# Optimization experiments

Measured on AMD Instinct MI355X. Metric: run time of the kernel, lower is better.

## Reference

```python
import jax, jax.numpy as jnp
import numpy as np

EPS = 1e-5

def conv1x1(x, w, b):
    # x: [B,C,H,W], w: [O,C], b: [O]
    return jnp.einsum('bchw,oc->bohw', x, w) + b[None, :, None, None]

def bn(x, gamma, beta, mean, var):
    scale = gamma / jnp.sqrt(var + EPS)
    return x * scale[None, :, None, None] + (beta - mean * scale)[None, :, None, None]

def setup_inputs() -> dict:
    B, C, H, W = 8, 256, 64, 64
    F0, F1 = 128, 128
    key = jax.random.key(0)
    ks = jax.random.split(key, 16)
    d = {}
    d['inputs'] = jax.random.normal(ks[0], (B, C, H, W), dtype=jnp.float32)
    def make_cna(i, fout, fin):
        w = jax.random.normal(ks[i], (fout, fin), dtype=jnp.float32) / np.sqrt(fin)
        b = jnp.zeros((fout,), dtype=jnp.float32)
        g = jnp.ones((fout,), dtype=jnp.float32)
        be = jnp.zeros((fout,), dtype=jnp.float32)
        m = 0.1 * jax.random.normal(ks[i + 1], (fout,), dtype=jnp.float32)
        v = jax.random.uniform(ks[i + 2], (fout,), dtype=jnp.float32, minval=0.5, maxval=1.5)
        return w, b, g, be, m, v
    (d['theta_w'], d['theta_b'], d['theta_g'], d['theta_beta'], d['theta_m'], d['theta_v']) = make_cna(1, F0, C)
    (d['phi_w'], d['phi_b'], d['phi_g'], d['phi_beta'], d['phi_m'], d['phi_v']) = make_cna(4, F0, C)
    (d['mu_w'], d['mu_b'], d['mu_g'], d['mu_beta'], d['mu_m'], d['mu_v']) = make_cna(7, F1, C)
    d['pre_w'] = jax.random.normal(ks[10], (C, F1), dtype=jnp.float32) / np.sqrt(F1)
    d['pre_b'] = jnp.zeros((C,), dtype=jnp.float32)
    d['post_g'] = jnp.ones((C,), dtype=jnp.float32)
    d['post_beta'] = jnp.zeros((C,), dtype=jnp.float32)
    d['post_m'] = 0.1 * jax.random.normal(ks[11], (C,), dtype=jnp.float32)
    d['post_v'] = jax.random.uniform(ks[12], (C,), dtype=jnp.float32, minval=0.5, maxval=1.5)
    return d

def reference(inputs, theta_w, theta_b, theta_g, theta_beta, theta_m, theta_v,
              phi_w, phi_b, phi_g, phi_beta, phi_m, phi_v,
              mu_w, mu_b, mu_g, mu_beta, mu_m, mu_v,
              pre_w, pre_b, post_g, post_beta, post_m, post_v):
    B, C, H, W = inputs.shape
    N = H * W
    # theta/phi/mu: 1x1 conv + batchnorm (eval) + relu
    t = jax.nn.relu(bn(conv1x1(inputs, theta_w, theta_b), theta_g, theta_beta, theta_m, theta_v))
    p = jax.nn.relu(bn(conv1x1(inputs, phi_w, phi_b), phi_g, phi_beta, phi_m, phi_v))
    z = jax.nn.relu(bn(conv1x1(inputs, mu_w, mu_b), mu_g, mu_beta, mu_m, mu_v))
    tf = t.reshape(B, -1, N)   # [B,F0,N]
    pf = p.reshape(B, -1, N)   # [B,F0,N]
    zf = z.reshape(B, -1, N)   # [B,F1,N]
    # unscaled softmax(theta^T phi) mu^T, batched (original loops over B)
    attn = jax.nn.softmax(jnp.einsum('bfn,bfm->bnm', tf, pf), axis=-1)  # [B,N,N]
    u = jnp.einsum('bnm,bfm->bfn', attn, zf).reshape(B, -1, H, W)       # [B,F1,H,W]
    pre = conv1x1(u, pre_w, pre_b)                                       # [B,C,H,W]
    return jax.nn.relu(bn(pre + inputs, post_g, post_beta, post_m, post_v))
```

## Files before the change

kernel.cpp:

```cpp
#include <hip/hip_runtime.h>

typedef __attribute__((ext_vector_type(8))) _Float16 f16x8;
typedef __attribute__((ext_vector_type(4))) float f32x4;

#define EPSV 1e-5f
#define BB 8
#define CC 256
#define NP 4096
#define FF 128
#define SPLIT 4
#define CHUNK 1024

static __device__ __forceinline__ unsigned short f2h(float f) {
    union { _Float16 h; unsigned short u; } v;
    v.h = (_Float16)f;
    return v.u;
}
static __device__ __forceinline__ float h2f(unsigned short u) {
    union { unsigned short u; _Float16 h; } v;
    v.u = u;
    return (float)v.h;
}

struct PrepArgs {
    const float* w[3]; const float* bias[3]; const float* g[3]; const float* be[3];
    const float* m[3]; const float* v[3];
    const float* pre_w; const float* pre_b;
    const float* post_g; const float* post_be; const float* post_m; const float* post_v;
    unsigned short* W_all; float* b_all; unsigned short* W2; float* b2; float* sres;
};

__global__ __launch_bounds__(256) void prep_kernel(PrepArgs a) {
    int idx = blockIdx.x * 256 + threadIdx.x;
    if (idx < 3 * 128 * 256) {
        int row = idx >> 8, c = idx & 255;
        int which = row >> 7, f = row & 127;
        float s = a.g[which][f] * rsqrtf(a.v[which][f] + EPSV);
        a.W_all[idx] = f2h(a.w[which][f * 256 + c] * s);
        if (c == 0)
            a.b_all[row] = s * a.bias[which][f] + a.be[which][f] - a.m[which][f] * s;
    } else {
        int i = idx - 3 * 128 * 256;
        if (i < 256 * 128) {
            int c = i >> 7, f = i & 127;
            float s = a.post_g[c] * rsqrtf(a.post_v[c] + EPSV);
            a.W2[i] = f2h(a.pre_w[i] * s);
            if (f == 0) {
                a.b2[c] = s * a.pre_b[c] + a.post_be[c] - a.post_m[c] * s;
                a.sres[c] = s;
            }
        }
    }
}

__global__ __launch_bounds__(256) void transpose_x_kernel(const float* __restrict__ x,
                                                          unsigned short* __restrict__ xT) {
    __shared__ float tile[64][65];
    int blk = blockIdx.x;
    int b  = blk >> 8;
    int c0 = ((blk >> 6) & 3) << 6;
    int n0 = (blk & 63) << 6;
    int t = threadIdx.x;
    const float* src = x + ((size_t)b * CC + c0) * NP + n0;
    #pragma unroll
    for (int i = 0; i < 16; ++i) {
        int cl = i * 4 + (t >> 6);
        tile[cl][t & 63] = src[(size_t)cl * NP + (t & 63)];
    }
    __syncthreads();
    unsigned short* dst = xT + ((size_t)b * NP + n0) * CC + c0;
    #pragma unroll
    for (int i = 0; i < 8; ++i) {
        int nl = i * 8 + (t >> 5);
        int cl = (t & 31) * 2;
        unsigned lo = f2h(tile[cl][nl]);
        unsigned hi = f2h(tile[cl + 1][nl]);
        *reinterpret_cast<unsigned*>(dst + (size_t)nl * CC + cl) = (hi << 16) | lo;
    }
}

__global__ __launch_bounds__(256) void qkv_kernel(const unsigned short* __restrict__ xT,
                                                  const unsigned short* __restrict__ W_all,
                                                  const float* __restrict__ b_all,
                                                  unsigned short* __restrict__ tq,
                                                  unsigned short* __restrict__ kp,
                                                  unsigned short* __restrict__ vz) {
    __shared__ unsigned short Alds[128 * 72];
    __shared__ unsigned short Blds[128 * 72];
    int blk = blockIdx.x;
    int b  = blk & 7;
    int r  = blk >> 3;
    int ft = r >> 5;
    int n0 = (r & 31) << 7;
    int fbase = ft << 7;
    int t = threadIdx.x, w = t >> 6, l = t & 63;
    int wr = (w >> 1) << 6, wc = (w & 1) << 6;
    const unsigned short* A  = xT + ((size_t)b * NP + n0) * CC;
    const unsigned short* Bw = W_all + (size_t)fbase * CC;

    f32x4 acc[4][4];
    #pragma unroll
    for (int i = 0; i < 4; ++i)
        #pragma unroll
        for (int j = 0; j < 4; ++j)
            acc[i][j] = f32x4{0.f, 0.f, 0.f, 0.f};

    for (int c0 = 0; c0 < 256; c0 += 64) {
        #pragma unroll
        for (int i = 0; i < 4; ++i) {
            int row = i * 32 + (t >> 3);
            int ch = (t & 7) * 8;
            *reinterpret_cast<int4*>(&Alds[row * 72 + ch]) =
                *reinterpret_cast<const int4*>(A + (size_t)row * CC + c0 + ch);
            *reinterpret_cast<int4*>(&Blds[row * 72 + ch]) =
                *reinterpret_cast<const int4*>(Bw + (size_t)row * CC + c0 + ch);
        }
        __syncthreads();
        #pragma unroll
        for (int kk = 0; kk < 2; ++kk) {
            f16x8 af[4], bfr[4];
            #pragma unroll
            for (int mi = 0; mi < 4; ++mi)
                af[mi] = *reinterpret_cast<const f16x8*>(
                    &Alds[(wr + mi * 16 + (l & 15)) * 72 + kk * 32 + (l >> 4) * 8]);
            #pragma unroll
            for (int ni = 0; ni < 4; ++ni)
                bfr[ni] = *reinterpret_cast<const f16x8*>(
                    &Blds[(wc + ni * 16 + (l & 15)) * 72 + kk * 32 + (l >> 4) * 8]);
            #pragma unroll
            for (int mi = 0; mi < 4; ++mi)
                #pragma unroll
                for (int ni = 0; ni < 4; ++ni)
                    acc[mi][ni] = __builtin_amdgcn_mfma_f32_16x16x32_f16(af[mi], bfr[ni], acc[mi][ni], 0, 0, 0);
        }
        __syncthreads();
    }

    #pragma unroll
    for (int mi = 0; mi < 4; ++mi) {
        #pragma unroll
        for (int ni = 0; ni < 4; ++ni) {
            int fl = wc + ni * 16 + (l & 15);
            float bias = b_all[fbase + fl];
            int nb = n0 + wr + mi * 16 + ((l >> 4) << 2);
            if (ft == 2) {
                unsigned pk0, pk1;
                float v0 = acc[mi][ni][0] + bias; v0 = v0 > 0.f ? v0 : 0.f;
                float v1 = acc[mi][ni][1] + bias; v1 = v1 > 0.f ? v1 : 0.f;
                float v2 = acc[mi][ni][2] + bias; v2 = v2 > 0.f ? v2 : 0.f;
                float v3 = acc[mi][ni][3] + bias; v3 = v3 > 0.f ? v3 : 0.f;
                pk0 = (unsigned)f2h(v0) | ((unsigned)f2h(v1) << 16);
                pk1 = (unsigned)f2h(v2) | ((unsigned)f2h(v3) << 16);
                uint2 uu; uu.x = pk0; uu.y = pk1;
                *reinterpret_cast<uint2*>(vz + (size_t)b * FF * NP + (size_t)fl * NP + nb) = uu;
            } else {
                unsigned short* dst = (ft == 0 ? tq : kp) + (size_t)b * NP * FF;
                #pragma unroll
                for (int rg = 0; rg < 4; ++rg) {
                    float v = acc[mi][ni][rg] + bias;
                    dst[(size_t)(nb + rg) * FF + fl] = f2h(v > 0.f ? v : 0.f);
                }
            }
        }
    }
}

__global__ __launch_bounds__(256, 4) void attn_kernel(const unsigned short* __restrict__ tq,
                                                      const unsigned short* __restrict__ kp,
                                                      const unsigned short* __restrict__ vz,
                                                      unsigned short* __restrict__ Uh,
                                                      float2* __restrict__ ml) {
    __shared__ unsigned short Klds[32 * 136];
    __shared__ unsigned short Vlds[128 * 40];
    __shared__ unsigned short Plds[4][32 * 40];
    int blk = blockIdx.x;
    int b = blk & 7;
    int rest = blk >> 3;
    int s = rest & 3;
    int qt = rest >> 2;
    int t = threadIdx.x, w = t >> 6, l = t & 63;
    int n0 = qt * 128 + w * 32;
    int mbase = s * CHUNK;
    const unsigned short* Q = tq + (size_t)b * NP * FF;
    const unsigned short* K = kp + (size_t)b * NP * FF;
    const unsigned short* V = vz + (size_t)b * FF * NP;

    f16x8 qa[2][4];
    #pragma unroll
    for (int g = 0; g < 2; ++g)
        #pragma unroll
        for (int kk = 0; kk < 4; ++kk)
            qa[g][kk] = *reinterpret_cast<const f16x8*>(
                Q + (size_t)(n0 + g * 16 + (l & 15)) * FF + kk * 32 + (l >> 4) * 8);

    f32x4 U[2][8];
    float mrun[2], lrun[2];
    #pragma unroll
    for (int g = 0; g < 2; ++g) {
        #pragma unroll
        for (int fb = 0; fb < 8; ++fb) U[g][fb] = f32x4{0.f, 0.f, 0.f, 0.f};
        mrun[g] = -1e30f; lrun[g] = 0.f;
    }

    int sm = t >> 3, sch = (t & 7) * 8;
    int sf = t >> 2, smm = (t & 3) * 8;

    for (int it = 0; it < CHUNK / 32; ++it) {
        int m0 = mbase + it * 32;
        int4 ka  = *reinterpret_cast<const int4*>(K + (size_t)(m0 + sm) * FF + sch);
        int4 kb2 = *reinterpret_cast<const int4*>(K + (size_t)(m0 + sm) * FF + 64 + sch);
        int4 va  = *reinterpret_cast<const int4*>(V + (size_t)sf * NP + m0 + smm);
        int4 vb2 = *reinterpret_cast<const int4*>(V + (size_t)(sf + 64) * NP + m0 + smm);
        *reinterpret_cast<int4*>(&Klds[sm * 136 + sch]) = ka;
        *reinterpret_cast<int4*>(&Klds[sm * 136 + 64 + sch]) = kb2;
        *reinterpret_cast<int2*>(&Vlds[sf * 40 + smm])            = make_int2(va.x, va.y);
        *reinterpret_cast<int2*>(&Vlds[sf * 40 + smm + 4])        = make_int2(va.z, va.w);
        *reinterpret_cast<int2*>(&Vlds[(sf + 64) * 40 + smm])     = make_int2(vb2.x, vb2.y);
        *reinterpret_cast<int2*>(&Vlds[(sf + 64) * 40 + smm + 4]) = make_int2(vb2.z, vb2.w);
        __syncthreads();

        f32x4 St[2][2];
        #pragma unroll
        for (int mt = 0; mt < 2; ++mt) {
            St[mt][0] = f32x4{0.f, 0.f, 0.f, 0.f};
            St[mt][1] = f32x4{0.f, 0.f, 0.f, 0.f};
        }
        __builtin_amdgcn_s_setprio(1);
        #pragma unroll
        for (int mt = 0; mt < 2; ++mt)
            #pragma unroll
            for (int kk = 0; kk < 4; ++kk) {
                f16x8 kf = *reinterpret_cast<const f16x8*>(
                    &Klds[(mt * 16 + (l & 15)) * 136 + kk * 32 + (l >> 4) * 8]);
                St[mt][0] = __builtin_amdgcn_mfma_f32_16x16x32_f16(kf, qa[0][kk], St[mt][0], 0, 0, 0);
                St[mt][1] = __builtin_amdgcn_mfma_f32_16x16x32_f16(kf, qa[1][kk], St[mt][1], 0, 0, 0);
            }
        __builtin_amdgcn_s_setprio(0);

        #pragma unroll
        for (int g = 0; g < 2; ++g) {
            float pmax = St[0][g][0];
            pmax = fmaxf(pmax, St[0][g][1]); pmax = fmaxf(pmax, St[0][g][2]);
            pmax = fmaxf(pmax, St[0][g][3]); pmax = fmaxf(pmax, St[1][g][0]);
            pmax = fmaxf(pmax, St[1][g][1]); pmax = fmaxf(pmax, St[1][g][2]);
            pmax = fmaxf(pmax, St[1][g][3]);
            pmax = fmaxf(pmax, __shfl_xor(pmax, 16));
            pmax = fmaxf(pmax, __shfl_xor(pmax, 32));
            if (__any(pmax > mrun[g] + 8.0f)) {
                float mnew = fmaxf(mrun[g], pmax);
                float sc = __expf(mrun[g] - mnew);
                mrun[g] = mnew;
                lrun[g] *= sc;
                #pragma unroll
                for (int rg = 0; rg < 4; ++rg) {
                    float scu = __shfl(sc, ((l >> 4) << 2) | rg);
                    #pragma unroll
                    for (int fb = 0; fb < 8; ++fb) U[g][fb][rg] *= scu;
                }
            }
            float lsum = 0.f;
            #pragma unroll
            for (int mt = 0; mt < 2; ++mt)
                #pragma unroll
                for (int rg = 0; rg < 4; ++rg) {
                    float p = __expf(St[mt][g][rg] - mrun[g]);
                    St[mt][g][rg] = p;
                    lsum += p;
                }
            lsum += __shfl_xor(lsum, 16);
            lsum += __shfl_xor(lsum, 32);
            lrun[g] += lsum;
            #pragma unroll
            for (int mt = 0; mt < 2; ++mt) {
                unsigned p01 = (unsigned)f2h(St[mt][g][0]) | ((unsigned)f2h(St[mt][g][1]) << 16);
                unsigned p23 = (unsigned)f2h(St[mt][g][2]) | ((unsigned)f2h(St[mt][g][3]) << 16);
                int base = (g * 16 + (l & 15)) * 40 + mt * 16 + ((l >> 4) << 2);
                *reinterpret_cast<unsigned*>(&Plds[w][base])     = p01;
                *reinterpret_cast<unsigned*>(&Plds[w][base + 2]) = p23;
            }
        }

        f16x8 pa[2];
        #pragma unroll
        for (int g = 0; g < 2; ++g)
            pa[g] = *reinterpret_cast<const f16x8*>(
                &Plds[w][(g * 16 + (l & 15)) * 40 + (l >> 4) * 8]);
        __builtin_amdgcn_s_setprio(1);
        #pragma unroll
        for (int fb = 0; fb < 8; ++fb) {
            f16x8 vf = *reinterpret_cast<const f16x8*>(
                &Vlds[(fb * 16 + (l & 15)) * 40 + (l >> 4) * 8]);
            U[0][fb] = __builtin_amdgcn_mfma_f32_16x16x32_f16(pa[0], vf, U[0][fb], 0, 0, 0);
            U[1][fb] = __builtin_amdgcn_mfma_f32_16x16x32_f16(pa[1], vf, U[1][fb], 0, 0, 0);
        }
        __builtin_amdgcn_s_setprio(0);
        __syncthreads();
    }

    unsigned short* up = Uh + (size_t)(s * 8 + b) * NP * FF;
    #pragma unroll
    for (int g = 0; g < 2; ++g) {
        float linv = 1.0f / lrun[g];
        #pragma unroll
        for (int rg = 0; rg < 4; ++rg) {
            float li = __shfl(linv, ((l >> 4) << 2) | rg);
            int n = n0 + g * 16 + ((l >> 4) << 2) + rg;
            #pragma unroll
            for (int fb = 0; fb < 8; ++fb)
                up[(size_t)n * FF + fb * 16 + (l & 15)] = f2h(U[g][fb][rg] * li);
        }
    }
    if (l < 16) {
        ml[(size_t)(s * 8 + b) * NP + n0 + l]      = make_float2(mrun[0], lrun[0]);
        ml[(size_t)(s * 8 + b) * NP + n0 + 16 + l] = make_float2(mrun[1], lrun[1]);
    }
}

__global__ __launch_bounds__(256) void combine_kernel(const unsigned short* __restrict__ Uh,
                                                      const float2* __restrict__ ml,
                                                      unsigned short* __restrict__ uT) {
    int row = blockIdx.x * 2 + (threadIdx.x >> 7);
    int f = threadIdx.x & 127;
    float m[SPLIT], lv[SPLIT];
    #pragma unroll
    for (int s = 0; s < SPLIT; ++s) {
        float2 v = ml[(size_t)s * (BB * NP) + row];
        m[s] = v.x; lv[s] = v.y;
    }
    float M = fmaxf(fmaxf(m[0], m[1]), fmaxf(m[2], m[3]));
    float wsum = 0.f, acc = 0.f;
    #pragma unroll
    for (int s = 0; s < SPLIT; ++s) {
        float wgt = __expf(m[s] - M) * lv[s];
        wsum += wgt;
        acc += wgt * h2f(Uh[((size_t)s * (BB * NP) + row) * FF + f]);
    }
    uT[(size_t)row * FF + f] = f2h(acc / wsum);
}

__global__ __launch_bounds__(256) void final_kernel(const unsigned short* __restrict__ uT,
                                                    const unsigned short* __restrict__ W2,
                                                    const float* __restrict__ b2,
                                                    const float* __restrict__ sres,
                                                    const float* __restrict__ x,
                                                    float* __restrict__ out) {
    __shared__ unsigned short Alds[128 * 72];
    __shared__ unsigned short Blds[128 * 72];
    int blk = blockIdx.x;
    int b  = blk & 7;
    int r  = blk >> 3;
    int ct = r & 1;
    int nt = r >> 1;
    int c0 = ct << 7, n0 = nt << 7;
    int t = threadIdx.x, w = t >> 6, l = t & 63;
    int wr = (w >> 1) << 6, wc = (w & 1) << 6;

    f32x4 acc[4][4];
    #pragma unroll
    for (int i = 0; i < 4; ++i)
        #pragma unroll
        for (int j = 0; j < 4; ++j)
            acc[i][j] = f32x4{0.f, 0.f, 0.f, 0.f};

    for (int k0 = 0; k0 < 128; k0 += 64) {
        #pragma unroll
        for (int i = 0; i < 4; ++i) {
            int row = i * 32 + (t >> 3);
            int ch = (t & 7) * 8;
            *reinterpret_cast<int4*>(&Alds[row * 72 + ch]) =
                *reinterpret_cast<const int4*>(W2 + (size_t)(c0 + row) * FF + k0 + ch);
            *reinterpret_cast<int4*>(&Blds[row * 72 + ch]) =
                *reinterpret_cast<const int4*>(uT + ((size_t)b * NP + n0 + row) * FF + k0 + ch);
        }
        __syncthreads();
        #pragma unroll
        for (int kk = 0; kk < 2; ++kk) {
            f16x8 af[4], bfr[4];
            #pragma unroll
            for (int mi = 0; mi < 4; ++mi)
                af[mi] = *reinterpret_cast<const f16x8*>(
                    &Alds[(wr + mi * 16 + (l & 15)) * 72 + kk * 32 + (l >> 4) * 8]);
            #pragma unroll
            for (int ni = 0; ni < 4; ++ni)
                bfr[ni] = *reinterpret_cast<const f16x8*>(
                    &Blds[(wc + ni * 16 + (l & 15)) * 72 + kk * 32 + (l >> 4) * 8]);
            #pragma unroll
            for (int mi = 0; mi < 4; ++mi)
                #pragma unroll
                for (int ni = 0; ni < 4; ++ni)
                    acc[mi][ni] = __builtin_amdgcn_mfma_f32_16x16x32_f16(af[mi], bfr[ni], acc[mi][ni], 0, 0, 0);
        }
        __syncthreads();
    }

    const float* xb = x + (size_t)b * CC * NP;
    float* ob = out + (size_t)b * CC * NP;
    #pragma unroll
    for (int mi = 0; mi < 4; ++mi)
        #pragma unroll
        for (int ni = 0; ni < 4; ++ni) {
            int n = n0 + wc + ni * 16 + (l & 15);
            int cb = c0 + wr + mi * 16 + ((l >> 4) << 2);
            #pragma unroll
            for (int rg = 0; rg < 4; ++rg) {
                int c = cb + rg;
                float v = acc[mi][ni][rg] + b2[c] + sres[c] * xb[(size_t)c * NP + n];
                ob[(size_t)c * NP + n] = v > 0.f ? v : 0.f;
            }
        }
}

extern "C" void kernel_launch(void* const* d_in, const int* in_sizes, int n_in,
                              void* d_out, int out_size, void* d_ws, size_t ws_size,
                              hipStream_t stream) {
    const float* x = (const float*)d_in[0];
    char* ws = (char*)d_ws;
    unsigned short* W_all = (unsigned short*)(ws);
    float*          b_all = (float*)(ws + 196608);
    unsigned short* W2    = (unsigned short*)(ws + 198144);
    float*          b2    = (float*)(ws + 263680);
    float*          sres  = (float*)(ws + 264704);
    unsigned short* xT    = (unsigned short*)(ws + 265728);
    unsigned short* tq    = (unsigned short*)(ws + 17042944);
    unsigned short* kp    = (unsigned short*)(ws + 25431552);
    unsigned short* vz    = (unsigned short*)(ws + 33820160);
    unsigned short* uT    = (unsigned short*)(ws + 42208768);
    unsigned short* Uh    = (unsigned short*)(ws + 50597376);
    float2*         ml    = (float2*)(ws + 84151808);

    PrepArgs pa;
    pa.w[0]  = (const float*)d_in[1];  pa.bias[0] = (const float*)d_in[2];
    pa.g[0]  = (const float*)d_in[3];  pa.be[0]   = (const float*)d_in[4];
    pa.m[0]  = (const float*)d_in[5];  pa.v[0]    = (const float*)d_in[6];
    pa.w[1]  = (const float*)d_in[7];  pa.bias[1] = (const float*)d_in[8];
    pa.g[1]  = (const float*)d_in[9];  pa.be[1]   = (const float*)d_in[10];
    pa.m[1]  = (const float*)d_in[11]; pa.v[1]    = (const float*)d_in[12];
    pa.w[2]  = (const float*)d_in[13]; pa.bias[2] = (const float*)d_in[14];
    pa.g[2]  = (const float*)d_in[15]; pa.be[2]   = (const float*)d_in[16];
    pa.m[2]  = (const float*)d_in[17]; pa.v[2]    = (const float*)d_in[18];
    pa.pre_w = (const float*)d_in[19]; pa.pre_b   = (const float*)d_in[20];
    pa.post_g = (const float*)d_in[21]; pa.post_be = (const float*)d_in[22];
    pa.post_m = (const float*)d_in[23]; pa.post_v  = (const float*)d_in[24];
    pa.W_all = W_all; pa.b_all = b_all; pa.W2 = W2; pa.b2 = b2; pa.sres = sres;

    prep_kernel<<<dim3(512), dim3(256), 0, stream>>>(pa);
    transpose_x_kernel<<<dim3(2048), dim3(256), 0, stream>>>(x, xT);
    qkv_kernel<<<dim3(768), dim3(256), 0, stream>>>(xT, W_all, b_all, tq, kp, vz);
    attn_kernel<<<dim3(1024), dim3(256), 0, stream>>>(tq, kp, vz, Uh, ml);
    combine_kernel<<<dim3(16384), dim3(256), 0, stream>>>(Uh, ml, uT);
    final_kernel<<<dim3(512), dim3(256), 0, stream>>>(uT, W2, b2, sres, x, (float*)d_out);
}
```

Before: 274.1 us.

## Rework flash-attention kernel with 32x32 MFMA, async LDS double buffering, register-resident P

Rewrites the attention inner loop to use 32x32x16 MFMA tiles instead of 16x16x32, keeping the softmax probabilities in registers and exchanging halves with cross-lane shuffles rather than going through shared memory. K/V tiles of 64 keys are loaded with global_load_lds directly into XOR-swizzled, double-buffered LDS, so the next tile is prefetched while the current one is computed. This removes one barrier per iteration and doubles the tile size. LDS use rises to 64KB per block and launch bounds drop to 2 blocks per CU, which reduces occupancy in exchange for less LDS traffic and more overlap.

Result: faster. 266.2 us (-2.9%).

```diff
diff --git a/kernel.cpp b/kernel.cpp
--- a/kernel.cpp
+++ b/kernel.cpp
@@ -2,6 +2,8 @@
 
 typedef __attribute__((ext_vector_type(8))) _Float16 f16x8;
 typedef __attribute__((ext_vector_type(4))) float f32x4;
+typedef __attribute__((ext_vector_type(16))) float f32x16;
+typedef __attribute__((ext_vector_type(4))) unsigned u32x4;
 
 #define EPSV 1e-5f
 #define BB 8
@@ -10,6 +12,11 @@
 #define FF 128
 #define SPLIT 4
 #define CHUNK 1024
+#define NIT 16
+
+#define GLD16(gp, lp) __builtin_amdgcn_global_load_lds( \
+    (const __attribute__((address_space(1))) unsigned int*)(gp), \
+    (__attribute__((address_space(3))) unsigned int*)(lp), 16, 0, 0)
 
 static __device__ __forceinline__ unsigned short f2h(float f) {
     union { _Float16 h; unsigned short u; } v;
@@ -165,155 +172,154 @@
     }
 }
 
-__global__ __launch_bounds__(256, 4) void attn_kernel(const unsigned short* __restrict__ tq,
+__global__ __launch_bounds__(256, 2) void attn_kernel(const unsigned short* __restrict__ tq,
                                                       const unsigned short* __restrict__ kp,
                                                       const unsigned short* __restrict__ vz,
                                                       unsigned short* __restrict__ Uh,
                                                       float2* __restrict__ ml) {
-    __shared__ unsigned short Klds[32 * 136];
-    __shared__ unsigned short Vlds[128 * 40];
-    __shared__ unsigned short Plds[4][32 * 40];
+    __shared__ unsigned short Kl[2][8192];
+    __shared__ unsigned short Vl[2][8192];
     int blk = blockIdx.x;
     int b = blk & 7;
     int rest = blk >> 3;
     int s = rest & 3;
     int qt = rest >> 2;
     int t = threadIdx.x, w = t >> 6, l = t & 63;
-    int n0 = qt * 128 + w * 32;
+    int r = l & 31, h = l >> 5, lx = l & 7;
+    int n0w = qt * 128 + w * 32;
     int mbase = s * CHUNK;
     const unsigned short* Q = tq + (size_t)b * NP * FF;
     const unsigned short* K = kp + (size_t)b * NP * FF;
     const unsigned short* V = vz + (size_t)b * FF * NP;
 
-    f16x8 qa[2][4];
-    #pragma unroll
-    for (int g = 0; g < 2; ++g)
-        #pragma unroll
-        for (int kk = 0; kk < 4; ++kk)
-            qa[g][kk] = *reinterpret_cast<const f16x8*>(
-                Q + (size_t)(n0 + g * 16 + (l & 15)) * FF + kk * 32 + (l >> 4) * 8);
-
-    f32x4 U[2][8];
-    float mrun[2], lrun[2];
-    #pragma unroll
-    for (int g = 0; g < 2; ++g) {
-        #pragma unroll
-        for (int fb = 0; fb < 8; ++fb) U[g][fb] = f32x4{0.f, 0.f, 0.f, 0.f};
-        mrun[g] = -1e30f; lrun[g] = 0.f;
-    }
-
-    int sm = t >> 3, sch = (t & 7) * 8;
-    int sf = t >> 2, smm = (t & 3) * 8;
-
-    for (int it = 0; it < CHUNK / 32; ++it) {
-        int m0 = mbase + it * 32;
-        int4 ka  = *reinterpret_cast<const int4*>(K + (size_t)(m0 + sm) * FF + sch);
-        int4 kb2 = *reinterpret_cast<const int4*>(K + (size_t)(m0 + sm) * FF + 64 + sch);
-        int4 va  = *reinterpret_cast<const int4*>(V + (size_t)sf * NP + m0 + smm);
-        int4 vb2 = *reinterpret_cast<const int4*>(V + (size_t)(sf + 64) * NP + m0 + smm);
-        *reinterpret_cast<int4*>(&Klds[sm * 136 + sch]) = ka;
-        *reinterpret_cast<int4*>(&Klds[sm * 136 + 64 + sch]) = kb2;
-        *reinterpret_cast<int2*>(&Vlds[sf * 40 + smm])            = make_int2(va.x, va.y);
-        *reinterpret_cast<int2*>(&Vlds[sf * 40 + smm + 4])        = make_int2(va.z, va.w);
-        *reinterpret_cast<int2*>(&Vlds[(sf + 64) * 40 + smm])     = make_int2(vb2.x, vb2.y);
-        *reinterpret_cast<int2*>(&Vlds[(sf + 64) * 40 + smm + 4]) = make_int2(vb2.z, vb2.w);
-        __syncthreads();
-
-        f32x4 St[2][2];
-        #pragma unroll
-        for (int mt = 0; mt < 2; ++mt) {
-            St[mt][0] = f32x4{0.f, 0.f, 0.f, 0.f};
-            St[mt][1] = f32x4{0.f, 0.f, 0.f, 0.f};
-        }
+    f16x8 qf[8];
+    #pragma unroll
+    for (int kf = 0; kf < 8; ++kf)
+        qf[kf] = *reinterpret_cast<const f16x8*>(Q + (size_t)(n0w + r) * FF + kf * 16 + h * 8);
+
+    f32x16 U[4];
+    #pragma unroll
+    for (int fb = 0; fb < 4; ++fb)
+        #pragma unroll
+        for (int i = 0; i < 16; ++i) U[fb][i] = 0.f;
+    float mrun = -1e30f, lrun = 0.f;
+
+    const unsigned short* kbase[4];
+    const unsigned short* vbase[4];
+    #pragma unroll
+    for (int i = 0; i < 4; ++i) {
+        int seg = w * 4 + i;
+        int krow = seg * 4 + (l >> 4);
+        kbase[i] = K + (size_t)(mbase + krow) * FF + 8 * ((l & 15) ^ (krow & 7));
+        int frow = seg * 8 + (l >> 3);
+        vbase[i] = V + (size_t)frow * NP + mbase + 8 * ((l & 7) ^ (frow & 7));
+    }
+
+    #pragma unroll
+    for (int i = 0; i < 4; ++i) {
+        GLD16(kbase[i], &Kl[0][(w * 4 + i) * 512]);
+        GLD16(vbase[i], &Vl[0][(w * 4 + i) * 512]);
+    }
+
+    int cur = 0;
+    for (int it = 0; it < NIT; ++it) {
+        asm volatile("s_waitcnt vmcnt(0)" ::: "memory");
+        __builtin_amdgcn_s_barrier();
+        asm volatile("" ::: "memory");
+        if (it + 1 < NIT) {
+            #pragma unroll
+            for (int i = 0; i < 4; ++i) {
+                GLD16(kbase[i] + (size_t)(it + 1) * 64 * FF, &Kl[cur ^ 1][(w * 4 + i) * 512]);
+                GLD16(vbase[i] + (it + 1) * 64, &Vl[cur ^ 1][(w * 4 + i) * 512]);
+            }
+        }
+        const unsigned short* Kb = Kl[cur];
+        const unsigned short* Vb = Vl[cur];
+
+        f32x16 St0, St1;
+        #pragma unroll
+        for (int i = 0; i < 16; ++i) { St0[i] = 0.f; St1[i] = 0.f; }
         __builtin_amdgcn_s_setprio(1);
         #pragma unroll
-        for (int mt = 0; mt < 2; ++mt)
-            #pragma unroll
-            for (int kk = 0; kk < 4; ++kk) {
-                f16x8 kf = *reinterpret_cast<const f16x8*>(
-                    &Klds[(mt * 16 + (l & 15)) * 136 + kk * 32 + (l >> 4) * 8]);
-                St[mt][0] = __builtin_amdgcn_mfma_f32_16x16x32_f16(kf, qa[0][kk], St[mt][0], 0, 0, 0);
-                St[mt][1] = __builtin_amdgcn_mfma_f32_16x16x32_f16(kf, qa[1][kk], St[mt][1], 0, 0, 0);
-            }
+        for (int kf = 0; kf < 8; ++kf) {
+            f16x8 a0 = *reinterpret_cast<const f16x8*>(Kb + r * 128 + 8 * ((2 * kf + h) ^ lx));
+            f16x8 a1 = *reinterpret_cast<const f16x8*>(Kb + (32 + r) * 128 + 8 * ((2 * kf + h) ^ lx));
+            St0 = __builtin_amdgcn_mfma_f32_32x32x16_f16(a0, qf[kf], St0, 0, 0, 0);
+            St1 = __builtin_amdgcn_mfma_f32_32x32x16_f16(a1, qf[kf], St1, 0, 0, 0);
+        }
         __builtin_amdgcn_s_setprio(0);
 
-        #pragma unroll
-        for (int g = 0; g < 2; ++g) {
-            float pmax = St[0][g][0];
-            pmax = fmaxf(pmax, St[0][g][1]); pmax = fmaxf(pmax, St[0][g][2]);
-            pmax = fmaxf(pmax, St[0][g][3]); pmax = fmaxf(pmax, St[1][g][0]);
-            pmax = fmaxf(pmax, St[1][g][1]); pmax = fmaxf(pmax, St[1][g][2]);
-            pmax = fmaxf(pmax, St[1][g][3]);
-            pmax = fmaxf(pmax, __shfl_xor(pmax, 16));
-            pmax = fmaxf(pmax, __shfl_xor(pmax, 32));
-            if (__any(pmax > mrun[g] + 8.0f)) {
-                float mnew = fmaxf(mrun[g], pmax);
-                float sc = __expf(mrun[g] - mnew);
-                mrun[g] = mnew;
-                lrun[g] *= sc;
-                #pragma unroll
-                for (int rg = 0; rg < 4; ++rg) {
-                    float scu = __shfl(sc, ((l >> 4) << 2) | rg);
-                    #pragma unroll
-                    for (int fb = 0; fb < 8; ++fb) U[g][fb][rg] *= scu;
-                }
-            }
-            float lsum = 0.f;
-            #pragma unroll
-            for (int mt = 0; mt < 2; ++mt)
-                #pragma unroll
-                for (int rg = 0; rg < 4; ++rg) {
-                    float p = __expf(St[mt][g][rg] - mrun[g]);
-                    St[mt][g][rg] = p;
-                    lsum += p;
-                }
-            lsum += __shfl_xor(lsum, 16);
-            lsum += __shfl_xor(lsum, 32);
-            lrun[g] += lsum;
-            #pragma unroll
-            for (int mt = 0; mt < 2; ++mt) {
-                unsigned p01 = (unsigned)f2h(St[mt][g][0]) | ((unsigned)f2h(St[mt][g][1]) << 16);
-                unsigned p23 = (unsigned)f2h(St[mt][g][2]) | ((unsigned)f2h(St[mt][g][3]) << 16);
-                int base = (g * 16 + (l & 15)) * 40 + mt * 16 + ((l >> 4) << 2);
-                *reinterpret_cast<unsigned*>(&Plds[w][base])     = p01;
-                *reinterpret_cast<unsigned*>(&Plds[w][base + 2]) = p23;
-            }
-        }
-
-        f16x8 pa[2];
-        #pragma unroll
-        for (int g = 0; g < 2; ++g)
-            pa[g] = *reinterpret_cast<const f16x8*>(
-                &Plds[w][(g * 16 + (l & 15)) * 40 + (l >> 4) * 8]);
+        float pmax = St0[0];
+        #pragma unroll
+        for (int i = 1; i < 16; ++i) pmax = fmaxf(pmax, St0[i]);
+        #pragma unroll
+        for (int i = 0; i < 16; ++i) pmax = fmaxf(pmax, St1[i]);
+        pmax = fmaxf(pmax, __shfl_xor(pmax, 32));
+        if (__any(pmax > mrun + 8.0f)) {
+            float mnew = fmaxf(mrun, pmax);
+            float sc = __expf(mrun - mnew);
+            mrun = mnew; lrun *= sc;
+            #pragma unroll
+            for (int rr = 0; rr < 16; ++rr) {
+                float scb = __shfl(sc, (rr & 3) + 8 * (rr >> 2) + 4 * h);
+                U[0][rr] *= scb; U[1][rr] *= scb; U[2][rr] *= scb; U[3][rr] *= scb;
+            }
+        }
+        float lsum = 0.f;
+        unsigned pka[8], pkb[8];
+        #pragma unroll
+        for (int rr = 0; rr < 8; ++rr) {
+            float e0 = __expf(St0[2 * rr] - mrun);
+            float e1 = __expf(St0[2 * rr + 1] - mrun);
+            float e2 = __expf(St1[2 * rr] - mrun);
+            float e3 = __expf(St1[2 * rr + 1] - mrun);
+            lsum += (e0 + e1) + (e2 + e3);
+            pka[rr] = __builtin_bit_cast(unsigned, __builtin_amdgcn_cvt_pkrtz(e0, e1));
+            pkb[rr] = __builtin_bit_cast(unsigned, __builtin_amdgcn_cvt_pkrtz(e2, e3));
+        }
+        lsum += __shfl_xor(lsum, 32);
+        lrun += lsum;
+
         __builtin_amdgcn_s_setprio(1);
         #pragma unroll
-        for (int fb = 0; fb < 8; ++fb) {
-            f16x8 vf = *reinterpret_cast<const f16x8*>(
-                &Vlds[(fb * 16 + (l & 15)) * 40 + (l >> 4) * 8]);
-            U[0][fb] = __builtin_amdgcn_mfma_f32_16x16x32_f16(pa[0], vf, U[0][fb], 0, 0, 0);
-            U[1][fb] = __builtin_amdgcn_mfma_f32_16x16x32_f16(pa[1], vf, U[1][fb], 0, 0, 0);
+        for (int kb = 0; kb < 4; ++kb) {
+            int ib = 4 * (kb & 1);
+            unsigned p0 = (kb < 2) ? pka[ib + 0] : pkb[ib + 0];
+            unsigned p1 = (kb < 2) ? pka[ib + 1] : pkb[ib + 1];
+            unsigned p2 = (kb < 2) ? pka[ib + 2] : pkb[ib + 2];
+            unsigned p3 = (kb < 2) ? pka[ib + 3] : pkb[ib + 3];
+            unsigned x0 = __shfl_xor(p0, 32), x1 = __shfl_xor(p1, 32);
+            unsigned y0 = __shfl_xor(p2, 32), y1 = __shfl_xor(p3, 32);
+            u32x4 du;
+            du[0] = h ? y0 : p0;
+            du[1] = h ? y1 : p1;
+            du[2] = h ? p2 : x0;
+            du[3] = h ? p3 : x1;
+            f16x8 af = __builtin_bit_cast(f16x8, du);
+            #pragma unroll
+            for (int fb = 0; fb < 4; ++fb) {
+                f16x8 vf = *reinterpret_cast<const f16x8*>(
+                    Vb + (fb * 32 + r) * 64 + 8 * ((2 * kb + h) ^ lx));
+                U[fb] = __builtin_amdgcn_mfma_f32_32x32x16_f16(af, vf, U[fb], 0, 0, 0);
+            }
         }
         __builtin_amdgcn_s_setprio(0);
-        __syncthreads();
-    }
-
+        cur ^= 1;
+    }
+
+    float linv = 1.0f / lrun;
     unsigned short* up = Uh + (size_t)(s * 8 + b) * NP * FF;
     #pragma unroll
-    for (int g = 0; g < 2; ++g) {
-        float linv = 1.0f / lrun[g];
-        #pragma unroll
-        for (int rg = 0; rg < 4; ++rg) {
-            float li = __shfl(linv, ((l >> 4) << 2) | rg);
-            int n = n0 + g * 16 + ((l >> 4) << 2) + rg;
-            #pragma unroll
-            for (int fb = 0; fb < 8; ++fb)
-                up[(size_t)n * FF + fb * 16 + (l & 15)] = f2h(U[g][fb][rg] * li);
-        }
-    }
-    if (l < 16) {
-        ml[(size_t)(s * 8 + b) * NP + n0 + l]      = make_float2(mrun[0], lrun[0]);
-        ml[(size_t)(s * 8 + b) * NP + n0 + 16 + l] = make_float2(mrun[1], lrun[1]);
-    }
+    for (int rr = 0; rr < 16; ++rr) {
+        int nn = (rr & 3) + 8 * (rr >> 2) + 4 * h;
+        float scb = __shfl(linv, nn);
+        int n = n0w + nn;
+        #pragma unroll
+        for (int fb = 0; fb < 4; ++fb)
+            up[(size_t)n * FF + fb * 32 + r] = f2h(U[fb][rr] * scb);
+    }
+    if (l < 32)
+        ml[(size_t)(s * 8 + b) * NP + n0w + l] = make_float2(mrun, lrun);
 }
 
 __global__ __launch_bounds__(256) void combine_kernel(const unsigned short* __restrict__ Uh,
```
